# Optimization experiments

Measured on AMD Instinct MI355X. Metric: run time of the kernel, lower is better.

## Reference

```python
import jax, jax.numpy as jnp
import numpy as np

NUM_HEADS = 8


def setup_inputs() -> dict:
    key = jax.random.key(0)
    ks = jax.random.split(key, 5)
    b, c, h, w = 8, 256, 32, 32
    x = jax.random.normal(ks[0], (b, c, h, w), dtype=jnp.float32)
    w_qkv = jax.random.normal(ks[1], (3 * c, c), dtype=jnp.float32) * (c ** -0.5)
    b_qkv = jax.random.normal(ks[2], (3 * c,), dtype=jnp.float32) * 0.02
    w_proj = jax.random.normal(ks[3], (c, c), dtype=jnp.float32) * (c ** -0.5)
    b_proj = jax.random.normal(ks[4], (c,), dtype=jnp.float32) * 0.02
    return {"x": x, "w_qkv": w_qkv, "b_qkv": b_qkv, "w_proj": w_proj, "b_proj": b_proj}


def reference(x, w_qkv, b_qkv, w_proj, b_proj):
    b, c, h, w = x.shape
    nh = NUM_HEADS
    dh = c // nh
    L = h * w
    scale = dh ** -0.5
    # 1x1 conv == per-pixel GEMM
    qkv = jnp.einsum('bchw,oc->bohw', x, w_qkv) + b_qkv[None, :, None, None]
    qkv = qkv.reshape(b, 3, nh, dh, L)
    q, k, v = qkv[:, 0], qkv[:, 1], qkv[:, 2]  # each (b, nh, dh, L)
    attn = jnp.einsum('bhdi,bhdj->bhij', q, k) * scale  # (b, nh, L, L)
    attn = jax.nn.softmax(attn, axis=-1)
    out = jnp.einsum('bhdj,bhij->bhdi', v, attn)  # (b, nh, dh, L)
    out = out.reshape(b, c, h, w)
    proj = jnp.einsum('bchw,oc->bohw', out, w_proj) + b_proj[None, :, None, None]
    return x + proj
```

## Files before the change

kernel.cpp:

```cpp
#include <hip/hip_runtime.h>
#include <math.h>

#define B_   8
#define CIN  256
#define L_   1024
#define NH_  8
#define DH_  32

typedef __attribute__((ext_vector_type(8))) short short8;
typedef __attribute__((ext_vector_type(4))) short short4v;
typedef __attribute__((ext_vector_type(4))) float f32x4;
typedef __attribute__((ext_vector_type(4))) unsigned int uint4v;
typedef __attribute__((ext_vector_type(2))) unsigned int uint2v;

__device__ inline short f2bf_hu(float f) {
    union { float f; unsigned u; } v; v.f = f;
    return (short)((v.u + 0x8000u) >> 16);
}
__device__ inline unsigned pkbf2(float a, float b) {
    union { float f; unsigned u; } x, y; x.f = a; y.f = b;
    return __builtin_amdgcn_perm(y.u + 0x8000u, x.u + 0x8000u, 0x07060302u);
}

__global__ __launch_bounds__(256) void qkv_gemm(
    const float* __restrict__ x, const float* __restrict__ w,
    const float* __restrict__ bias, short* __restrict__ qkvT)
{
    __shared__ short Xs[64][40];
    __shared__ short Wt[128][40];
    const int t = threadIdx.x, lane = t & 63, wv = t >> 6;
    const int n = lane & 15, quad = lane >> 4;
    const int b = blockIdx.z, o0 = blockIdx.y * 128, l0 = blockIdx.x * 64;

    float bias_r[8];
    #pragma unroll
    for (int nf = 0; nf < 8; nf++) bias_r[nf] = bias[o0 + nf * 16 + n];

    f32x4 acc[8];
    #pragma unroll
    for (int nf = 0; nf < 8; nf++) acc[nf] = (f32x4){0.f, 0.f, 0.f, 0.f};

    const int cS = t >> 3, lsS = (t & 7) * 8;
    const int rslot = ((cS >> 3) << 3) | (cS & 7);

    for (int c0 = 0; c0 < CIN; c0 += 32) {
        {
            const float* xp = &x[(((size_t)b * CIN + c0 + cS) << 10) + l0 + lsS];
            const float4 xa = *(const float4*)xp;
            const float4 xb = *(const float4*)(xp + 4);
            const float vals[8] = {xa.x, xa.y, xa.z, xa.w, xb.x, xb.y, xb.z, xb.w};
            #pragma unroll
            for (int k = 0; k < 8; k++) {
                const int l = lsS + k;
                const int col = (((cS >> 3) ^ (l & 3)) << 3) | (cS & 7);
                Xs[l][col] = f2bf_hu(vals[k]);
            }
        }
        {
            const int o = t >> 1, cs = (t & 1) * 16;
            const float* wp = &w[(size_t)(o0 + o) * CIN + c0 + cs];
            const float4 w0 = *(const float4*)(wp);
            const float4 w1 = *(const float4*)(wp + 4);
            const float4 w2 = *(const float4*)(wp + 8);
            const float4 w3 = *(const float4*)(wp + 12);
            uint4v pa = { pkbf2(w0.x, w0.y), pkbf2(w0.z, w0.w),
                          pkbf2(w1.x, w1.y), pkbf2(w1.z, w1.w) };
            uint4v pb = { pkbf2(w2.x, w2.y), pkbf2(w2.z, w2.w),
                          pkbf2(w3.x, w3.y), pkbf2(w3.z, w3.w) };
            *(uint4v*)&Wt[o][cs]     = pa;
            *(uint4v*)&Wt[o][cs + 8] = pb;
        }
        __syncthreads();

        const int arow = wv * 16 + n;
        const short8 af = *(const short8*)&Xs[arow][(quad ^ (arow & 3)) * 8];
        #pragma unroll
        for (int nf = 0; nf < 8; nf++) {
            const short8 bf = *(const short8*)&Wt[nf * 16 + n][quad * 8];
            acc[nf] = __builtin_amdgcn_mfma_f32_16x16x32_bf16(af, bf, acc[nf], 0, 0, 0);
        }
        __syncthreads();
    }

    #pragma unroll
    for (int reg = 0; reg < 4; reg++) {
        const size_t l = l0 + wv * 16 + quad * 4 + reg;
        short* row = qkvT + (((size_t)b << 10) + l) * 768 + o0 + n;
        #pragma unroll
        for (int nf = 0; nf < 8; nf++)
            row[nf * 16] = f2bf_hu(acc[nf][reg] + bias_r[nf]);
    }
}

__global__ __launch_bounds__(256) void proj_gemm(
    const short* __restrict__ aT, const float* __restrict__ w,
    const float* __restrict__ bias, const float* __restrict__ resid,
    float* __restrict__ out)
{
    __shared__ short Xs[64][40];
    __shared__ short Wt[64][40];
    const int t = threadIdx.x, lane = t & 63, wv = t >> 6;
    const int n = lane & 15, quad = lane >> 4;
    const int b = blockIdx.z, o0 = blockIdx.y * 64, l0 = blockIdx.x * 64;

    float bias_r[4];
    #pragma unroll
    for (int reg = 0; reg < 4; reg++) bias_r[reg] = bias[o0 + wv * 16 + quad * 4 + reg];

    f32x4 acc[4];
    #pragma unroll
    for (int nf = 0; nf < 4; nf++) acc[nf] = (f32x4){0.f, 0.f, 0.f, 0.f};

    for (int c0 = 0; c0 < CIN; c0 += 32) {
        {
            const int l = t >> 2, cs = (t & 3) * 8;
            *(uint4v*)&Xs[l][cs] =
                *(const uint4v*)&aT[(((size_t)b << 10) + l0 + l) * CIN + c0 + cs];
        }
        {
            const int o = t >> 2, cs = (t & 3) * 8;
            const float* wp = &w[(size_t)(o0 + o) * CIN + c0 + cs];
            const float4 a4 = *(const float4*)(wp);
            const float4 b4 = *(const float4*)(wp + 4);
            uint4v pw = { pkbf2(a4.x, a4.y), pkbf2(a4.z, a4.w),
                          pkbf2(b4.x, b4.y), pkbf2(b4.z, b4.w) };
            *(uint4v*)&Wt[o][cs] = pw;
        }
        __syncthreads();

        const short8 af = *(const short8*)&Wt[wv * 16 + n][quad * 8];
        #pragma unroll
        for (int nf = 0; nf < 4; nf++) {
            const short8 bf = *(const short8*)&Xs[nf * 16 + n][quad * 8];
            acc[nf] = __builtin_amdgcn_mfma_f32_16x16x32_bf16(af, bf, acc[nf], 0, 0, 0);
        }
        __syncthreads();
    }

    #pragma unroll
    for (int reg = 0; reg < 4; reg++) {
        const int o = o0 + wv * 16 + quad * 4 + reg;
        #pragma unroll
        for (int nf = 0; nf < 4; nf++) {
            const size_t off = (((size_t)b * CIN + o) << 10) + l0 + nf * 16 + n;
            out[off] = acc[nf][reg] + bias_r[reg] + resid[off];
        }
    }
}

__global__ __launch_bounds__(256) void attn_mfma(
    const short* __restrict__ qkvT, short* __restrict__ attnoT)
{
    __shared__ short Vt[2][32][80];
    __shared__ __align__(16) char umem[64 * 88 * 2];
    short (*Ss)[88] = (short(*)[88])umem;
    float (*OtT)[38] = (float(*)[38])umem;

    const int t = threadIdx.x, lane = t & 63, wv = t >> 6;
    const int n = lane & 15, quad = lane >> 4;
    const int b = blockIdx.z, h = blockIdx.y, i0 = blockIdx.x * 64;

    const short* base = qkvT + ((size_t)b << 10) * 768;
    const short* kbase = base + 256 + h * DH_;
    const short* vbase = base + 512 + h * DH_;

    const short8 qa = *(const short8*)&base[(size_t)(i0 + wv * 16 + n) * 768 + h * DH_ + quad * 8];

    short8 vf2;
    {
        const short one = (n == 0) ? (short)0x3F80 : (short)0;
        #pragma unroll
        for (int u = 0; u < 8; u++) vf2[u] = one;
    }

    f32x4 o_acc[3];
    #pragma unroll
    for (int nf = 0; nf < 3; nf++) o_acc[nf] = (f32x4){0.f, 0.f, 0.f, 0.f};

    const float K1 = 0.25503510f;
    const float K2 = 11.54156036f;

    const int jS = t >> 3, dsS = (t & 7) * 4;

    #pragma unroll
    for (int rr = 0; rr < 2; rr++) {
        const int j = jS + rr * 32;
        const short4v v4 = *(const short4v*)&vbase[(size_t)j * 768 + dsS];
        #pragma unroll
        for (int u = 0; u < 4; u++) {
            const int dv = dsS + u;
            Vt[0][dv][j ^ (((dv >> 2) & 7) << 3)] = v4[u];
        }
    }
    short8 kf[4];
    #pragma unroll
    for (int f = 0; f < 4; f++)
        kf[f] = *(const short8*)&kbase[(size_t)(f * 16 + n) * 768 + quad * 8];

    for (int it = 0; it < 16; it++) {
        const int cur = it & 1;
        __syncthreads();

        short8 kf_n[4];
        if (it < 15) {
            const int j0n = (it + 1) * 64;
            #pragma unroll
            for (int rr = 0; rr < 2; rr++) {
                const int j = jS + rr * 32;
                const short4v v4 = *(const short4v*)&vbase[(size_t)(j0n + j) * 768 + dsS];
                #pragma unroll
                for (int u = 0; u < 4; u++) {
                    const int dv = dsS + u;
                    Vt[cur ^ 1][dv][j ^ (((dv >> 2) & 7) << 3)] = v4[u];
                }
            }
            #pragma unroll
            for (int f = 0; f < 4; f++)
                kf_n[f] = *(const short8*)&kbase[(size_t)(j0n + f * 16 + n) * 768 + quad * 8];
        }

        #pragma unroll
        for (int f = 0; f < 4; f++) {
            f32x4 z = {0.f, 0.f, 0.f, 0.f};
            const f32x4 s = __builtin_amdgcn_mfma_f32_16x16x32_bf16(kf[f], qa, z, 0, 0, 0);
            const float p0 = exp2f(fmaf(s[0], K1, -K2));
            const float p1 = exp2f(fmaf(s[1], K1, -K2));
            const float p2 = exp2f(fmaf(s[2], K1, -K2));
            const float p3 = exp2f(fmaf(s[3], K1, -K2));
            uint2v pk = { pkbf2(p0, p1), pkbf2(p2, p3) };
            *(uint2v*)&Ss[wv * 16 + n][f * 16 + quad * 4] = pk;
        }

        #pragma unroll
        for (int kk = 0; kk < 2; kk++) {
            const short8 pf = *(const short8*)&Ss[wv * 16 + n][kk * 32 + quad * 8];
            #pragma unroll
            for (int nf = 0; nf < 2; nf++) {
                const int dv = nf * 16 + n;
                const int msk = ((dv >> 2) & 7) << 3;
                const short8 vf = *(const short8*)&Vt[cur][dv][(kk * 32 + quad * 8) ^ msk];
                o_acc[nf] = __builtin_amdgcn_mfma_f32_16x16x32_bf16(pf, vf, o_acc[nf], 0, 0, 0);
            }
            o_acc[2] = __builtin_amdgcn_mfma_f32_16x16x32_bf16(pf, vf2, o_acc[2], 0, 0, 0);
        }

        #pragma unroll
        for (int f = 0; f < 4; f++) kf[f] = kf_n[f];
    }

    __syncthreads();
    #pragma unroll
    for (int r = 0; r < 4; r++) {
        const float lv  = __shfl(o_acc[2][r], lane & 48, 64);
        const float inv = 1.f / lv;
        const int il = wv * 16 + quad * 4 + r;
        OtT[il][n]      = o_acc[0][r] * inv;
        OtT[il][16 + n] = o_acc[1][r] * inv;
    }
    __syncthreads();
    short* ob = attnoT + (((size_t)b << 10) + i0) * CIN + h * DH_;
    #pragma unroll
    for (int r = 0; r < 2; r++) {
        const int idx = t + r * 256;
        const int l = idx >> 3, cs = (idx & 7) * 4;
        uint2v pv;
        pv.x = pkbf2(OtT[l][cs],     OtT[l][cs + 1]);
        pv.y = pkbf2(OtT[l][cs + 2], OtT[l][cs + 3]);
        *(uint2v*)&ob[(size_t)l * CIN + cs] = pv;
    }
}

extern "C" void kernel_launch(void* const* d_in, const int* in_sizes, int n_in,
                              void* d_out, int out_size, void* d_ws, size_t ws_size,
                              hipStream_t stream) {
    const float* x      = (const float*)d_in[0];
    const float* w_qkv  = (const float*)d_in[1];
    const float* b_qkv  = (const float*)d_in[2];
    const float* w_proj = (const float*)d_in[3];
    const float* b_proj = (const float*)d_in[4];
    float* out = (float*)d_out;

    short* qkvT   = (short*)d_ws;
    short* attnoT = qkvT + (size_t)B_ * L_ * 768;

    qkv_gemm<<<dim3(16, 6, B_), 256, 0, stream>>>(x, w_qkv, b_qkv, qkvT);
    attn_mfma<<<dim3(16, NH_, B_), 256, 0, stream>>>(qkvT, attnoT);
    proj_gemm<<<dim3(16, 4, B_), 256, 0, stream>>>(attnoT, w_proj, b_proj, x, out);
}
```

Before: 129.6 us.

## Store V transposed and load attention V fragments directly from global

The QKV projection now writes Q/K into a compact 512-wide buffer and V into a per-head transposed [d][L] layout. The attention kernel loads V MFMA operands directly from global memory into registers with prefetch, removing the LDS transpose, double buffering and the per-iteration block barrier. The trade-off is that V stores in the projection GEMM become strided 2-byte writes, which are poorly coalesced.

```diff
diff --git a/kernel.cpp b/kernel.cpp
--- a/kernel.cpp
+++ b/kernel.cpp
@@ -24,7 +24,8 @@
 
 __global__ __launch_bounds__(256) void qkv_gemm(
     const float* __restrict__ x, const float* __restrict__ w,
-    const float* __restrict__ bias, short* __restrict__ qkvT)
+    const float* __restrict__ bias, short* __restrict__ qkT,
+    short* __restrict__ vT)
 {
     __shared__ short Xs[64][40];
     __shared__ short Wt[128][40];
@@ -41,7 +42,6 @@
     for (int nf = 0; nf < 8; nf++) acc[nf] = (f32x4){0.f, 0.f, 0.f, 0.f};
 
     const int cS = t >> 3, lsS = (t & 7) * 8;
-    const int rslot = ((cS >> 3) << 3) | (cS & 7);
 
     for (int c0 = 0; c0 < CIN; c0 += 32) {
         {
@@ -82,13 +82,26 @@
         __syncthreads();
     }
 
-    #pragma unroll
-    for (int reg = 0; reg < 4; reg++) {
-        const size_t l = l0 + wv * 16 + quad * 4 + reg;
-        short* row = qkvT + (((size_t)b << 10) + l) * 768 + o0 + n;
-        #pragma unroll
-        for (int nf = 0; nf < 8; nf++)
-            row[nf * 16] = f2bf_hu(acc[nf][reg] + bias_r[nf]);
+    if (o0 < 512) {
+        #pragma unroll
+        for (int reg = 0; reg < 4; reg++) {
+            const size_t l = l0 + wv * 16 + quad * 4 + reg;
+            short* row = qkT + ((((size_t)b << 10) + l) << 9) + o0 + n;
+            #pragma unroll
+            for (int nf = 0; nf < 8; nf++)
+                row[nf * 16] = f2bf_hu(acc[nf][reg] + bias_r[nf]);
+        }
+    } else {
+        #pragma unroll
+        for (int reg = 0; reg < 4; reg++) {
+            const size_t l = l0 + wv * 16 + quad * 4 + reg;
+            #pragma unroll
+            for (int nf = 0; nf < 8; nf++) {
+                const int ov = o0 - 512 + nf * 16 + n;
+                vT[(((size_t)(b << 3) << 5) + ov << 10) + l] =
+                    f2bf_hu(acc[nf][reg] + bias_r[nf]);
+            }
+        }
     }
 }
 
@@ -149,9 +162,9 @@
 }
 
 __global__ __launch_bounds__(256) void attn_mfma(
-    const short* __restrict__ qkvT, short* __restrict__ attnoT)
+    const short* __restrict__ qkT, const short* __restrict__ vT,
+    short* __restrict__ attnoT)
 {
-    __shared__ short Vt[2][32][80];
     __shared__ __align__(16) char umem[64 * 88 * 2];
     short (*Ss)[88] = (short(*)[88])umem;
     float (*OtT)[38] = (float(*)[38])umem;
@@ -160,11 +173,11 @@
     const int n = lane & 15, quad = lane >> 4;
     const int b = blockIdx.z, h = blockIdx.y, i0 = blockIdx.x * 64;
 
-    const short* base = qkvT + ((size_t)b << 10) * 768;
-    const short* kbase = base + 256 + h * DH_;
-    const short* vbase = base + 512 + h * DH_;
-
-    const short8 qa = *(const short8*)&base[(size_t)(i0 + wv * 16 + n) * 768 + h * DH_ + quad * 8];
+    const short* qbase = qkT + (((size_t)b << 10) << 9) + h * DH_;
+    const short* kbase = qbase + 256;
+    const short* vtb   = vT + ((size_t)((b << 3) + h) << 15);
+
+    const short8 qa = *(const short8*)&qbase[(size_t)(i0 + wv * 16 + n) << 9 | (quad * 8)];
 
     short8 vf2;
     {
@@ -180,43 +193,28 @@
     const float K1 = 0.25503510f;
     const float K2 = 11.54156036f;
 
-    const int jS = t >> 3, dsS = (t & 7) * 4;
-
-    #pragma unroll
-    for (int rr = 0; rr < 2; rr++) {
-        const int j = jS + rr * 32;
-        const short4v v4 = *(const short4v*)&vbase[(size_t)j * 768 + dsS];
-        #pragma unroll
-        for (int u = 0; u < 4; u++) {
-            const int dv = dsS + u;
-            Vt[0][dv][j ^ (((dv >> 2) & 7) << 3)] = v4[u];
-        }
-    }
-    short8 kf[4];
+    short8 kf[4], vf[2][2];
     #pragma unroll
     for (int f = 0; f < 4; f++)
-        kf[f] = *(const short8*)&kbase[(size_t)(f * 16 + n) * 768 + quad * 8];
+        kf[f] = *(const short8*)&kbase[(size_t)(f * 16 + n) << 9 | (quad * 8)];
+    #pragma unroll
+    for (int kk = 0; kk < 2; kk++)
+        #pragma unroll
+        for (int nf = 0; nf < 2; nf++)
+            vf[kk][nf] = *(const short8*)&vtb[((nf * 16 + n) << 10) + kk * 32 + quad * 8];
 
     for (int it = 0; it < 16; it++) {
-        const int cur = it & 1;
-        __syncthreads();
-
-        short8 kf_n[4];
+        short8 kf_n[4], vf_n[2][2];
         if (it < 15) {
             const int j0n = (it + 1) * 64;
             #pragma unroll
-            for (int rr = 0; rr < 2; rr++) {
-                const int j = jS + rr * 32;
-                const short4v v4 = *(const short4v*)&vbase[(size_t)(j0n + j) * 768 + dsS];
+            for (int f = 0; f < 4; f++)
+                kf_n[f] = *(const short8*)&kbase[(size_t)(j0n + f * 16 + n) << 9 | (quad * 8)];
+            #pragma unroll
+            for (int kk = 0; kk < 2; kk++)
                 #pragma unroll
-                for (int u = 0; u < 4; u++) {
-                    const int dv = dsS + u;
-                    Vt[cur ^ 1][dv][j ^ (((dv >> 2) & 7) << 3)] = v4[u];
-                }
-            }
-            #pragma unroll
-            for (int f = 0; f < 4; f++)
-                kf_n[f] = *(const short8*)&kbase[(size_t)(j0n + f * 16 + n) * 768 + quad * 8];
+                for (int nf = 0; nf < 2; nf++)
+                    vf_n[kk][nf] = *(const short8*)&vtb[((nf * 16 + n) << 10) + j0n + kk * 32 + quad * 8];
         }
 
         #pragma unroll
@@ -235,17 +233,17 @@
         for (int kk = 0; kk < 2; kk++) {
             const short8 pf = *(const short8*)&Ss[wv * 16 + n][kk * 32 + quad * 8];
             #pragma unroll
-            for (int nf = 0; nf < 2; nf++) {
-                const int dv = nf * 16 + n;
-                const int msk = ((dv >> 2) & 7) << 3;
-                const short8 vf = *(const short8*)&Vt[cur][dv][(kk * 32 + quad * 8) ^ msk];
-                o_acc[nf] = __builtin_amdgcn_mfma_f32_16x16x32_bf16(pf, vf, o_acc[nf], 0, 0, 0);
-            }
+            for (int nf = 0; nf < 2; nf++)
+                o_acc[nf] = __builtin_amdgcn_mfma_f32_16x16x32_bf16(pf, vf[kk][nf], o_acc[nf], 0, 0, 0);
             o_acc[2] = __builtin_amdgcn_mfma_f32_16x16x32_bf16(pf, vf2, o_acc[2], 0, 0, 0);
         }
 
         #pragma unroll
         for (int f = 0; f < 4; f++) kf[f] = kf_n[f];
+        #pragma unroll
+        for (int kk = 0; kk < 2; kk++)
+            #pragma unroll
+            for (int nf = 0; nf < 2; nf++) vf[kk][nf] = vf_n[kk][nf];
     }
 
     __syncthreads();
@@ -280,10 +278,11 @@
     const float* b_proj = (const float*)d_in[4];
     float* out = (float*)d_out;
 
-    short* qkvT   = (short*)d_ws;
-    short* attnoT = qkvT + (size_t)B_ * L_ * 768;
-
-    qkv_gemm<<<dim3(16, 6, B_), 256, 0, stream>>>(x, w_qkv, b_qkv, qkvT);
-    attn_mfma<<<dim3(16, NH_, B_), 256, 0, stream>>>(qkvT, attnoT);
+    short* qkT    = (short*)d_ws;
+    short* vT     = qkT + (size_t)B_ * L_ * 512;
+    short* attnoT = vT  + (size_t)B_ * CIN * L_;
+
+    qkv_gemm<<<dim3(16, 6, B_), 256, 0, stream>>>(x, w_qkv, b_qkv, qkT, vT);
+    attn_mfma<<<dim3(16, NH_, B_), 256, 0, stream>>>(qkT, vT, attnoT);
     proj_gemm<<<dim3(16, 4, B_), 256, 0, stream>>>(attnoT, w_proj, b_proj, x, out);
 }
```

Result: slower. 152.6 us (+17.7%).
